# Performance work log

Measured on AMD Instinct MI355X. Metric: run time of the kernel, lower is better.

Reference implementation:

```python
import jax, jax.numpy as jnp
import numpy as np

NUM_CONN = 8

def _ein_reduce(f):
    # Einstein t-norm fold over last axis: T(a,b) = ab / (2 - (a+b-ab))
    acc = f[..., 0]
    for i in range(1, f.shape[-1]):
        b = f[..., i]
        ab = acc * b
        acc = ab / (2.0 - (acc + b - ab))
    return acc

def _coein_reduce(f):
    # Einstein t-conorm fold over last axis: S(a,b) = (a+b) / (1 + ab)
    acc = f[..., 0]
    for i in range(1, f.shape[-1]):
        b = f[..., i]
        acc = (acc + b) / (1.0 + acc * b)
    return acc

def _ddlg_layer(x, w, idx, is_train):
    # x: [B, in], idx: [out, C] int, w: [out, 4]
    feats = x[:, idx]                      # [B, out, C] gather
    ops = jnp.stack([
        jnp.min(feats, axis=-1),
        jnp.max(feats, axis=-1),
        _ein_reduce(feats),
        _coein_reduce(feats),
    ], axis=-1)                            # [B, out, 4]
    if is_train:
        prob = jax.nn.softmax(w, axis=-1)  # [out, 4]
    else:
        prob = jax.nn.one_hot(jnp.argmax(w, axis=-1), 4, dtype=x.dtype)
    return jnp.einsum('bof,of->bo', ops, prob)

def setup_inputs() -> dict:
    key = jax.random.key(0)
    ks = jax.random.split(key, 6)
    sizes = [4096, 2048, 1024, 2048, 4096]
    x = jax.random.uniform(ks[0], (4096, sizes[0]), dtype=jnp.float32)
    ws = [jax.random.normal(ks[1 + i], (sizes[i + 1], 4), dtype=jnp.float32) for i in range(4)]
    rng = np.random.default_rng(0)
    idxs = []
    for i in range(4):
        # randperm-without-replacement per output neuron
        perm = np.argsort(rng.random((sizes[i + 1], sizes[i])), axis=-1)[:, :NUM_CONN]
        idxs.append(jnp.asarray(perm, dtype=jnp.int32))
    return {
        'x': x,
        'w0': ws[0], 'w1': ws[1], 'w2': ws[2], 'w3': ws[3],
        'idx0': idxs[0], 'idx1': idxs[1], 'idx2': idxs[2], 'idx3': idxs[3],
        'is_train': 1,
    }

def reference(x, w0, w1, w2, w3, idx0, idx1, idx2, idx3, is_train):
    h = _ddlg_layer(x, w0, idx0, is_train)
    h = _ddlg_layer(h, w1, idx1, is_train)
    h = _ddlg_layer(h, w2, idx2, is_train)
    h = _ddlg_layer(h, w3, idx3, is_train)
    return h
```

## Files before the change

### kernel.cpp

```cpp
#include <hip/hip_runtime.h>


#define BATCH 4096

typedef _Float16 h4 __attribute__((ext_vector_type(4)));

__device__ __forceinline__ float fastrcp(float x) { return __builtin_amdgcn_rcpf(x); }
__device__ __forceinline__ _Float16 hrcp(_Float16 x) {
#if __has_builtin(__builtin_amdgcn_rcph)
    return __builtin_amdgcn_rcph(x);
#else
    return (_Float16)__builtin_amdgcn_rcpf((float)x);
#endif
}
__device__ __forceinline__ h4 splat(_Float16 s) { h4 v = {s, s, s, s}; return v; }

__global__ __launch_bounds__(256) void prep_k(const float* __restrict__ w0,
                                              const float* __restrict__ w1,
                                              const float* __restrict__ w2,
                                              const float* __restrict__ w3,
                                              const int* __restrict__ is_train,
                                              h4* __restrict__ probsH) {
    const int g = blockIdx.x * 256 + threadIdx.x;
    const float* w; int o;
    if (g < 2048)      { w = w0; o = g; }
    else if (g < 3072) { w = w1; o = g - 2048; }
    else if (g < 5120) { w = w2; o = g - 3072; }
    else               { w = w3; o = g - 5120; }
    float wv[4];
#pragma unroll
    for (int c = 0; c < 4; ++c) wv[c] = w[(o << 2) + c];
    float p[4];
    if (*is_train) {
        float m = fmaxf(fmaxf(wv[0], wv[1]), fmaxf(wv[2], wv[3]));
        float s = 0.0f;
#pragma unroll
        for (int c = 0; c < 4; ++c) { p[c] = __expf(wv[c] - m); s += p[c]; }
        float inv = fastrcp(s);
#pragma unroll
        for (int c = 0; c < 4; ++c) p[c] *= inv;
    } else {
        int a = 0; float best = wv[0];
#pragma unroll
        for (int c = 1; c < 4; ++c) if (wv[c] > best) { best = wv[c]; a = c; }
#pragma unroll
        for (int c = 0; c < 4; ++c) p[c] = (c == a) ? 1.0f : 0.0f;
    }
    probsH[g] = h4{(_Float16)p[0], (_Float16)p[1], (_Float16)p[2], (_Float16)p[3]};
}

struct GatePre { int4 i0, i1; h4 P; };

__device__ __forceinline__ GatePre pre_load(const int4* __restrict__ idx,
                                            const h4* __restrict__ probs, int o) {
    GatePre g;
    g.i0 = idx[o * 2];
    g.i1 = idx[o * 2 + 1];
    g.P  = probs[o];
    return g;
}

__device__ __forceinline__ h4 gate_body(const h4* __restrict__ rows, const GatePre g) {
    h4 raw[8];
    raw[0] = rows[g.i0.x];
    raw[1] = rows[g.i0.y];
    raw[2] = rows[g.i0.z];
    raw[3] = rows[g.i0.w];
    raw[4] = rows[g.i1.x];
    raw[5] = rows[g.i1.y];
    raw[6] = rows[g.i1.z];
    raw[7] = rows[g.i1.w];

    const h4 one = splat((_Float16)1.0f);
    const h4 two = splat((_Float16)2.0f);

    h4 mn = raw[0], mx = raw[0], De = raw[0];
    h4 Ne = two - raw[0];
    h4 Nc = one + raw[0];
    h4 Dc = one - raw[0];
#pragma unroll
    for (int c = 1; c < 8; ++c) {
        h4 v = raw[c];
        mn = __builtin_elementwise_min(mn, v);
        mx = __builtin_elementwise_max(mx, v);
        De *= v;
        Ne *= (two - v);
        Nc += Nc * v;
        Dc -= Dc * v;
    }
    h4 s1 = Ne + De;
    h4 s2 = Nc + Dc;
    h4 d1 = Nc - Dc;
    h4 r1, r2;
#pragma unroll
    for (int e = 0; e < 4; ++e) { r1[e] = hrcp(s1[e]); r2[e] = hrcp(s2[e]); }
    h4 ein = (De + De) * r1;
    h4 coe = d1 * r2;
    h4 res = splat(g.P[0]) * mn;
    res += splat(g.P[1]) * mx;
    res += splat(g.P[2]) * ein;
    res += splat(g.P[3]) * coe;
    return res;
}

__global__ __launch_bounds__(1024, 8) void ddlg_fused(const float* __restrict__ x,
                                                      const h4* __restrict__ probsH,
                                                      const int4* __restrict__ idx0,
                                                      const int4* __restrict__ idx1,
                                                      const int4* __restrict__ idx2,
                                                      const int4* __restrict__ idx3,
                                                      float* __restrict__ out) {
    __shared__ __align__(16) _Float16 lds[24576];
    const int t  = threadIdx.x;
    const int b0 = blockIdx.x << 2;

    const h4* xl = (const h4*)lds;
    const h4* h0 = (const h4*)(lds + 16384);
    const h4* h1 = (const h4*)lds;
    const h4* h2 = (const h4*)(lds + 16384);

    GatePre gA = pre_load(idx0, probsH, t);
    GatePre gB = pre_load(idx0, probsH, t + 1024);

#pragma unroll
    for (int c = 0; c < 4; ++c) {
        const int j = (c << 10) + t;
        const float v0 = x[(size_t)(b0 + 0) * 4096 + j];
        const float v1 = x[(size_t)(b0 + 1) * 4096 + j];
        const float v2 = x[(size_t)(b0 + 2) * 4096 + j];
        const float v3 = x[(size_t)(b0 + 3) * 4096 + j];
        h4 hv;
        hv[0] = (_Float16)v0; hv[1] = (_Float16)v1;
        hv[2] = (_Float16)v2; hv[3] = (_Float16)v3;
        *(h4*)(lds + (j << 2)) = hv;
    }
    __syncthreads();

    {
        h4 r = gate_body(xl, gA);
        gA = pre_load(idx1, probsH + 2048, t);
        *(h4*)(lds + 16384 + (t << 2)) = r;
        r = gate_body(xl, gB);
        gB = pre_load(idx2, probsH + 3072, t);
        *(h4*)(lds + 16384 + ((t + 1024) << 2)) = r;
    }
    __syncthreads();

    {
        h4 r = gate_body(h0, gA);
        gA = pre_load(idx2, probsH + 3072, t + 1024);
        *(h4*)(lds + (t << 2)) = r;
    }
    __syncthreads();

    {
        h4 r = gate_body(h1, gB);
        gB = pre_load(idx3, probsH + 5120, t);
        *(h4*)(lds + 16384 + (t << 2)) = r;
        r = gate_body(h1, gA);
        gA = pre_load(idx3, probsH + 5120, t + 1024);
        *(h4*)(lds + 16384 + ((t + 1024) << 2)) = r;
    }
    __syncthreads();

    {
        h4 r = gate_body(h2, gB);
        gB = pre_load(idx3, probsH + 5120, t + 2048);
#pragma unroll
        for (int b = 0; b < 4; ++b)
            out[(size_t)(b0 + b) * 4096 + t] = (float)r[b];

        r = gate_body(h2, gA);
        gA = pre_load(idx3, probsH + 5120, t + 3072);
#pragma unroll
        for (int b = 0; b < 4; ++b)
            out[(size_t)(b0 + b) * 4096 + (t + 1024)] = (float)r[b];

        r = gate_body(h2, gB);
#pragma unroll
        for (int b = 0; b < 4; ++b)
            out[(size_t)(b0 + b) * 4096 + (t + 2048)] = (float)r[b];

        r = gate_body(h2, gA);
#pragma unroll
        for (int b = 0; b < 4; ++b)
            out[(size_t)(b0 + b) * 4096 + (t + 3072)] = (float)r[b];
    }
}

extern "C" void kernel_launch(void* const* d_in, const int* in_sizes, int n_in,
                              void* d_out, int out_size, void* d_ws, size_t ws_size,
                              hipStream_t stream) {
    const float* x        = (const float*)d_in[0];
    const float* w0       = (const float*)d_in[1];
    const float* w1       = (const float*)d_in[2];
    const float* w2       = (const float*)d_in[3];
    const float* w3       = (const float*)d_in[4];
    const int4*  idx0     = (const int4*)d_in[5];
    const int4*  idx1     = (const int4*)d_in[6];
    const int4*  idx2     = (const int4*)d_in[7];
    const int4*  idx3     = (const int4*)d_in[8];
    const int*   is_train = (const int*)d_in[9];
    float*       out      = (float*)d_out;

    h4* probsH = (h4*)d_ws;

    prep_k<<<36, 256, 0, stream>>>(w0, w1, w2, w3, is_train, probsH);
    ddlg_fused<<<1024, 1024, 0, stream>>>(x, probsH, idx0, idx1, idx2, idx3, out);
}
```

Measured before the change: 165.1 us.

## Assign adjacent gates per thread, vectorize stores, merge reciprocals into one

Each thread now computes adjacent output gates (2 or 4 consecutive) instead of gates strided by 1024. This allows 16-byte LDS stores and float4 global output stores in place of scalar strided ones. The two fp16 reciprocals per gate are merged into a single reciprocal of the product s1*s2, and the cross-layer prefetch of indices and probabilities is removed. The combined reciprocal risks fp16 overflow or precision loss, and dropping the prefetch may expose index-load latency.

```diff
diff --git a/kernel.cpp b/kernel.cpp
--- a/kernel.cpp
+++ b/kernel.cpp
@@ -49,59 +49,75 @@
     probsH[g] = h4{(_Float16)p[0], (_Float16)p[1], (_Float16)p[2], (_Float16)p[3]};
 }
 
-struct GatePre { int4 i0, i1; h4 P; };
-
-__device__ __forceinline__ GatePre pre_load(const int4* __restrict__ idx,
-                                            const h4* __restrict__ probs, int o) {
-    GatePre g;
-    g.i0 = idx[o * 2];
-    g.i1 = idx[o * 2 + 1];
-    g.P  = probs[o];
-    return g;
-}
-
-__device__ __forceinline__ h4 gate_body(const h4* __restrict__ rows, const GatePre g) {
-    h4 raw[8];
-    raw[0] = rows[g.i0.x];
-    raw[1] = rows[g.i0.y];
-    raw[2] = rows[g.i0.z];
-    raw[3] = rows[g.i0.w];
-    raw[4] = rows[g.i1.x];
-    raw[5] = rows[g.i1.y];
-    raw[6] = rows[g.i1.z];
-    raw[7] = rows[g.i1.w];
-
-    const h4 one = splat((_Float16)1.0f);
-    const h4 two = splat((_Float16)2.0f);
-
-    h4 mn = raw[0], mx = raw[0], De = raw[0];
-    h4 Ne = two - raw[0];
-    h4 Nc = one + raw[0];
-    h4 Dc = one - raw[0];
+struct Chain { h4 mn, mx, De, Ne, Nc, Dc; };
+
+__device__ __forceinline__ void chain_init(Chain& C, h4 v, h4 one, h4 two) {
+    C.mn = v; C.mx = v; C.De = v;
+    C.Ne = two - v; C.Nc = one + v; C.Dc = one - v;
+}
+__device__ __forceinline__ void chain_step(Chain& C, h4 v, h4 two) {
+    C.mn = __builtin_elementwise_min(C.mn, v);
+    C.mx = __builtin_elementwise_max(C.mx, v);
+    C.De *= v;
+    C.Ne *= (two - v);
+    C.Nc += C.Nc * v;
+    C.Dc -= C.Dc * v;
+}
+__device__ __forceinline__ h4 finale(const Chain& C, h4 P) {
+    h4 s1 = C.Ne + C.De;
+    h4 s2 = C.Nc + C.Dc;
+    h4 d1 = C.Nc - C.Dc;
+    h4 ss = s1 * s2;
+    h4 r;
+#pragma unroll
+    for (int e = 0; e < 4; ++e) r[e] = hrcp(ss[e]);
+    h4 t1 = (C.De + C.De) * s2;
+    h4 t2 = d1 * s1;
+    h4 num = splat(P[2]) * t1 + splat(P[3]) * t2;
+    return splat(P[0]) * C.mn + splat(P[1]) * C.mx + num * r;
+}
+
+__device__ __forceinline__ h4 gate1(const h4* __restrict__ rows,
+                                    const int4* __restrict__ idx,
+                                    const h4* __restrict__ probs, int o) {
+    const int4 i0 = idx[o * 2], i1 = idx[o * 2 + 1];
+    const h4 P = probs[o];
+    h4 A[8];
+    A[0] = rows[i0.x]; A[1] = rows[i0.y]; A[2] = rows[i0.z]; A[3] = rows[i0.w];
+    A[4] = rows[i1.x]; A[5] = rows[i1.y]; A[6] = rows[i1.z]; A[7] = rows[i1.w];
+    const h4 one = splat((_Float16)1.0f), two = splat((_Float16)2.0f);
+    Chain C; chain_init(C, A[0], one, two);
+#pragma unroll
+    for (int c = 1; c < 8; ++c) chain_step(C, A[c], two);
+    return finale(C, P);
+}
+
+__device__ __forceinline__ void gate2(const h4* __restrict__ rows,
+                                      const int4* __restrict__ idx,
+                                      const h4* __restrict__ probs,
+                                      int o0, h4& ra, h4& rb) {
+    const int4 a0 = idx[o0 * 2],     a1 = idx[o0 * 2 + 1];
+    const int4 b0 = idx[o0 * 2 + 2], b1 = idx[o0 * 2 + 3];
+    const h4 PA = probs[o0], PB = probs[o0 + 1];
+    h4 A[8], B[8];
+    A[0] = rows[a0.x]; A[1] = rows[a0.y]; A[2] = rows[a0.z]; A[3] = rows[a0.w];
+    A[4] = rows[a1.x]; A[5] = rows[a1.y]; A[6] = rows[a1.z]; A[7] = rows[a1.w];
+    B[0] = rows[b0.x]; B[1] = rows[b0.y]; B[2] = rows[b0.z]; B[3] = rows[b0.w];
+    B[4] = rows[b1.x]; B[5] = rows[b1.y]; B[6] = rows[b1.z]; B[7] = rows[b1.w];
+    const h4 one = splat((_Float16)1.0f), two = splat((_Float16)2.0f);
+    Chain CA, CB;
+    chain_init(CA, A[0], one, two);
+    chain_init(CB, B[0], one, two);
 #pragma unroll
     for (int c = 1; c < 8; ++c) {
-        h4 v = raw[c];
-        mn = __builtin_elementwise_min(mn, v);
-        mx = __builtin_elementwise_max(mx, v);
-        De *= v;
-        Ne *= (two - v);
-        Nc += Nc * v;
-        Dc -= Dc * v;
-    }
-    h4 s1 = Ne + De;
-    h4 s2 = Nc + Dc;
-    h4 d1 = Nc - Dc;
-    h4 r1, r2;
-#pragma unroll
-    for (int e = 0; e < 4; ++e) { r1[e] = hrcp(s1[e]); r2[e] = hrcp(s2[e]); }
-    h4 ein = (De + De) * r1;
-    h4 coe = d1 * r2;
-    h4 res = splat(g.P[0]) * mn;
-    res += splat(g.P[1]) * mx;
-    res += splat(g.P[2]) * ein;
-    res += splat(g.P[3]) * coe;
-    return res;
-}
+        chain_step(CA, A[c], two);
+        chain_step(CB, B[c], two);
+    }
+    ra = finale(CA, PA);
+    rb = finale(CB, PB);
+}
+
+struct alignas(16) H4x2 { h4 a, b; };
 
 __global__ __launch_bounds__(1024, 8) void ddlg_fused(const float* __restrict__ x,
                                                       const h4* __restrict__ probsH,
@@ -114,13 +130,10 @@
     const int t  = threadIdx.x;
     const int b0 = blockIdx.x << 2;
 
-    const h4* xl = (const h4*)lds;
-    const h4* h0 = (const h4*)(lds + 16384);
-    const h4* h1 = (const h4*)lds;
-    const h4* h2 = (const h4*)(lds + 16384);
-
-    GatePre gA = pre_load(idx0, probsH, t);
-    GatePre gB = pre_load(idx0, probsH, t + 1024);
+    const h4* xl  = (const h4*)lds;
+    const h4* h0v = (const h4*)(lds + 16384);
+    const h4* h1v = (const h4*)lds;
+    const h4* h2v = (const h4*)(lds + 16384);
 
 #pragma unroll
     for (int c = 0; c < 4; ++c) {
@@ -137,54 +150,35 @@
     __syncthreads();
 
     {
-        h4 r = gate_body(xl, gA);
-        gA = pre_load(idx1, probsH + 2048, t);
-        *(h4*)(lds + 16384 + (t << 2)) = r;
-        r = gate_body(xl, gB);
-        gB = pre_load(idx2, probsH + 3072, t);
-        *(h4*)(lds + 16384 + ((t + 1024) << 2)) = r;
-    }
-    __syncthreads();
-
-    {
-        h4 r = gate_body(h0, gA);
-        gA = pre_load(idx2, probsH + 3072, t + 1024);
+        h4 ra, rb;
+        gate2(xl, idx0, probsH, 2 * t, ra, rb);
+        *(H4x2*)(lds + 16384 + (t << 3)) = H4x2{ra, rb};
+    }
+    __syncthreads();
+
+    {
+        h4 r = gate1(h0v, idx1, probsH + 2048, t);
         *(h4*)(lds + (t << 2)) = r;
     }
     __syncthreads();
 
     {
-        h4 r = gate_body(h1, gB);
-        gB = pre_load(idx3, probsH + 5120, t);
-        *(h4*)(lds + 16384 + (t << 2)) = r;
-        r = gate_body(h1, gA);
-        gA = pre_load(idx3, probsH + 5120, t + 1024);
-        *(h4*)(lds + 16384 + ((t + 1024) << 2)) = r;
-    }
-    __syncthreads();
-
-    {
-        h4 r = gate_body(h2, gB);
-        gB = pre_load(idx3, probsH + 5120, t + 2048);
-#pragma unroll
-        for (int b = 0; b < 4; ++b)
-            out[(size_t)(b0 + b) * 4096 + t] = (float)r[b];
-
-        r = gate_body(h2, gA);
-        gA = pre_load(idx3, probsH + 5120, t + 3072);
-#pragma unroll
-        for (int b = 0; b < 4; ++b)
-            out[(size_t)(b0 + b) * 4096 + (t + 1024)] = (float)r[b];
-
-        r = gate_body(h2, gB);
-#pragma unroll
-        for (int b = 0; b < 4; ++b)
-            out[(size_t)(b0 + b) * 4096 + (t + 2048)] = (float)r[b];
-
-        r = gate_body(h2, gA);
-#pragma unroll
-        for (int b = 0; b < 4; ++b)
-            out[(size_t)(b0 + b) * 4096 + (t + 3072)] = (float)r[b];
+        h4 ra, rb;
+        gate2(h1v, idx2, probsH + 3072, 2 * t, ra, rb);
+        *(H4x2*)(lds + 16384 + (t << 3)) = H4x2{ra, rb};
+    }
+    __syncthreads();
+
+    {
+        h4 r0, r1, r2, r3;
+        gate2(h2v, idx3, probsH + 5120, 4 * t,     r0, r1);
+        gate2(h2v, idx3, probsH + 5120, 4 * t + 2, r2, r3);
+#pragma unroll
+        for (int b = 0; b < 4; ++b) {
+            float4 o4 = make_float4((float)r0[b], (float)r1[b],
+                                    (float)r2[b], (float)r3[b]);
+            *(float4*)(out + (size_t)(b0 + b) * 4096 + (t << 2)) = o4;
+        }
     }
 }
 
```

Result: no change. 164.2 us (-0.6%).
